# Optimization experiments

Hardware: AMD Instinct MI355X
Metric: run time of the kernel (lower is better)

The kernel has to match this reference:

```python
import math
import jax, jax.numpy as jnp
import numpy as np

B, S, D = 2, 2048, 4096
H, KVH = 32, 8
HD = D // H            # 128
REP = H // KVH         # 4


def setup_inputs() -> dict:
    key = jax.random.key(0)
    ks = jax.random.split(key, 7)
    scale = 1.0 / math.sqrt(D)
    return {
        "x": jax.random.normal(ks[0], (B, S, D), dtype=jnp.float32),
        "freqs_cos": jax.random.uniform(ks[1], (S, HD // 2), dtype=jnp.float32),
        "freqs_sin": jax.random.uniform(ks[2], (S, HD // 2), dtype=jnp.float32),
        "Wq": jax.random.normal(ks[3], (D, H * HD), dtype=jnp.float32) * scale,
        "Wk": jax.random.normal(ks[4], (D, KVH * HD), dtype=jnp.float32) * scale,
        "Wv": jax.random.normal(ks[5], (D, KVH * HD), dtype=jnp.float32) * scale,
        "Wo": jax.random.normal(ks[6], (H * HD, D), dtype=jnp.float32) * scale,
    }


def _rope(t, cos, sin):
    # t: [B,S,h,HD]; pairs are interleaved (reshape to (HD//2, 2) in original)
    tr = t[..., 0::2]
    ti = t[..., 1::2]
    cos = cos[None, :, None, :]  # [1,S,1,HD//2]
    sin = sin[None, :, None, :]
    out_r = tr * cos - ti * sin
    out_i = tr * sin + ti * cos
    return jnp.stack([out_r, out_i], axis=-1).reshape(t.shape)


def reference(x, freqs_cos, freqs_sin, Wq, Wk, Wv, Wo):
    b, s, _ = x.shape
    xq = (x @ Wq).reshape(b, s, H, HD)
    xk = (x @ Wk).reshape(b, s, KVH, HD)
    xv = (x @ Wv).reshape(b, s, KVH, HD)

    xq = _rope(xq, freqs_cos, freqs_sin)
    xk = _rope(xk, freqs_cos, freqs_sin)

    # GQA: repeat each kv head REP times -> [b,s,H,HD]
    xk = jnp.repeat(xk, REP, axis=2)
    xv = jnp.repeat(xv, REP, axis=2)

    q = xq.transpose(0, 2, 1, 3)  # [b,H,s,HD]
    k = xk.transpose(0, 2, 1, 3)
    v = xv.transpose(0, 2, 1, 3)

    scores = jnp.einsum('bhqd,bhkd->bhqk', q, k) / math.sqrt(HD)
    causal = jnp.tril(jnp.ones((s, s), dtype=bool))
    scores = jnp.where(causal[None, None], scores, jnp.float32(-jnp.inf))
    probs = jax.nn.softmax(scores.astype(jnp.float32), axis=-1).astype(x.dtype)

    out = jnp.einsum('bhqk,bhkd->bhqd', probs, v)
    out = out.transpose(0, 2, 1, 3).reshape(b, s, H * HD)
    return out @ Wo
```

## Files before the change

kernel.cpp:

```cpp
#include <hip/hip_runtime.h>

typedef unsigned short u16;
typedef unsigned int u32;
typedef __attribute__((ext_vector_type(8))) short bf16x8;
typedef __attribute__((ext_vector_type(8))) unsigned short u16x8;
typedef __attribute__((ext_vector_type(4))) unsigned short u16x4;
typedef __attribute__((ext_vector_type(4))) float f32x4;
typedef __attribute__((ext_vector_type(4))) unsigned int u32x4;

#define S_LEN 2048
#define NB 2
#define NH 32
#define NKVH 8
#define HD 128
#define DMODEL 4096
#define NEG_BIG (-1.0e30f)

__device__ __forceinline__ float bf2f(u16 x) {
  union { u32 u; float f; } v; v.u = ((u32)x) << 16; return v.f;
}
__device__ __forceinline__ u16 f2bf(float f) {
  union { float f; u32 u; } v; v.f = f;
  u32 r = v.u + 0x7FFFu + ((v.u >> 16) & 1u);
  return (u16)(r >> 16);
}

__device__ __forceinline__ void gload16(const void* g, void* l) {
  __builtin_amdgcn_global_load_lds(
      (const __attribute__((address_space(1))) void*)g,
      (__attribute__((address_space(3))) void*)l, 16, 0, 0);
}

__global__ __launch_bounds__(256) void convert_x(const float* __restrict__ x,
                                                 u16* __restrict__ xb)
{
  int i = blockIdx.x * 256 + threadIdx.x;
  f32x4 a = *(const f32x4*)&x[(size_t)i * 8];
  f32x4 b = *(const f32x4*)&x[(size_t)i * 8 + 4];
  u16x8 h = { f2bf(a[0]), f2bf(a[1]), f2bf(a[2]), f2bf(a[3]),
              f2bf(b[0]), f2bf(b[1]), f2bf(b[2]), f2bf(b[3]) };
  *(u16x8*)&xb[(size_t)i * 8] = h;
}

__global__ __launch_bounds__(256) void transpose_w(const float* __restrict__ W,
                                                   u16* __restrict__ out,
                                                   int N)
{
  __shared__ u16 Ls[64 * 68];
  const int t  = threadIdx.x;
  const int k0 = blockIdx.x * 64;
  const int n0 = blockIdx.y * 64;
#pragma unroll
  for (int i = 0; i < 4; ++i) {
    int kr = (t >> 4) + i * 16;
    int nc = (t & 15) * 4;
    f32x4 v = *(const f32x4*)&W[(size_t)(k0 + kr) * N + n0 + nc];
    u16x4 h = { f2bf(v[0]), f2bf(v[1]), f2bf(v[2]), f2bf(v[3]) };
    *(u16x4*)&Ls[kr * 68 + nc] = h;
  }
  __syncthreads();
#pragma unroll
  for (int i = 0; i < 2; ++i) {
    int nr = (t >> 3) + i * 32;
    int kc = (t & 7) * 8;
    u16x8 h;
#pragma unroll
    for (int j = 0; j < 8; ++j) h[j] = Ls[(kc + j) * 68 + nr];
    *(u16x8*)&out[(size_t)(n0 + nr) * 4096 + k0 + kc] = h;
  }
}

__global__ __launch_bounds__(256) void transpose_v(const u16* __restrict__ Yv,
                                                   u16* __restrict__ Vt)
{
  __shared__ u16 Ls[64 * 68];
  const int t  = threadIdx.x;
  const int s0 = blockIdx.x * 64;
  const int d0 = blockIdx.y * 64;
  const int z  = blockIdx.z;
#pragma unroll
  for (int i = 0; i < 2; ++i) {
    int sr = (t >> 3) + i * 32;
    int dc = (t & 7) * 8;
    u16x8 v = *(const u16x8*)&Yv[((size_t)(z >> 3) * S_LEN + s0 + sr) * 1024 +
                                 (z & 7) * 128 + d0 + dc];
    u16x4 lo = { v[0], v[1], v[2], v[3] };
    u16x4 hi = { v[4], v[5], v[6], v[7] };
    *(u16x4*)&Ls[sr * 68 + dc]     = lo;
    *(u16x4*)&Ls[sr * 68 + dc + 4] = hi;
  }
  __syncthreads();
#pragma unroll
  for (int i = 0; i < 2; ++i) {
    int dr = (t >> 3) + i * 32;
    int sc = (t & 7) * 8;
    u16x8 h;
#pragma unroll
    for (int j = 0; j < 8; ++j) h[j] = Ls[(sc + j) * 68 + dr];
    *(u16x8*)&Vt[((size_t)z * 128 + d0 + dr) * S_LEN + s0 + sc] = h;
  }
}

__global__ __launch_bounds__(256) void gemm_qkv(const u16* __restrict__ A,
                                                const u16* __restrict__ Bt,
                                                u16* __restrict__ Yq,
                                                u16* __restrict__ Yk,
                                                u16* __restrict__ Yv)
{
  __shared__ u16 As[128 * 64];
  __shared__ u16 Bs[128 * 64];
  const int tid  = threadIdx.x;
  const int wave = tid >> 6;
  const int lane = tid & 63;
  const int lr   = lane & 15;
  const int quad = lane >> 4;
  const int wm   = (wave >> 1) * 64;
  const int wn   = (wave & 1) * 64;
  const int bm   = blockIdx.y * 128;
  const int bn   = blockIdx.x * 128;

  const int col = (((lane & 7) ^ (lane >> 3)) * 8);
  const int r0  = wave * 32 + (lane >> 3);

  const f32x4 zero = {0.f, 0.f, 0.f, 0.f};
  f32x4 acc[4][4];
#pragma unroll
  for (int i = 0; i < 4; ++i)
#pragma unroll
    for (int j = 0; j < 4; ++j) acc[i][j] = zero;

  for (int kt = 0; kt < 4096; kt += 64) {
    __syncthreads();
#pragma unroll
    for (int c = 0; c < 4; ++c) {
      gload16(&A [(size_t)(bm + r0 + c * 8) * 4096 + kt + col],
              &As[wave * 2048 + c * 512]);
      gload16(&Bt[(size_t)(bn + r0 + c * 8) * 4096 + kt + col],
              &Bs[wave * 2048 + c * 512]);
    }
    __syncthreads();

#pragma unroll
    for (int kk = 0; kk < 2; ++kk) {
      bf16x8 af[4], bfr[4];
#pragma unroll
      for (int mt = 0; mt < 4; ++mt)
        af[mt] = *(const bf16x8*)&As[(wm + mt * 16 + lr) * 64 +
                                     (((kk * 4 + quad) ^ (lr & 7)) * 8)];
#pragma unroll
      for (int nt = 0; nt < 4; ++nt)
        bfr[nt] = *(const bf16x8*)&Bs[(wn + nt * 16 + lr) * 64 +
                                      (((kk * 4 + quad) ^ (lr & 7)) * 8)];
#pragma unroll
      for (int mt = 0; mt < 4; ++mt)
#pragma unroll
        for (int nt = 0; nt < 4; ++nt)
          acc[mt][nt] = __builtin_amdgcn_mfma_f32_16x16x32_bf16(af[mt], bfr[nt], acc[mt][nt], 0, 0, 0);
    }
  }

  u16* dst; size_t ldc; int nbase;
  if (bn < 4096)      { dst = Yq; ldc = 4096; nbase = bn; }
  else if (bn < 5120) { dst = Yk; ldc = 1024; nbase = bn - 4096; }
  else                { dst = Yv; ldc = 1024; nbase = bn - 5120; }
#pragma unroll
  for (int mt = 0; mt < 4; ++mt)
#pragma unroll
    for (int nt = 0; nt < 4; ++nt)
#pragma unroll
      for (int r = 0; r < 4; ++r) {
        size_t m = (size_t)(bm + wm + mt * 16 + quad * 4 + r);
        size_t n = (size_t)(nbase + wn + nt * 16 + lr);
        dst[m * ldc + n] = f2bf(acc[mt][nt][r]);
      }
}

__global__ __launch_bounds__(256) void gemm_o(const u16* __restrict__ A,
                                              const u16* __restrict__ Bt,
                                              float* __restrict__ C)
{
  __shared__ u16 As[128 * 64];
  __shared__ u16 Bs[128 * 64];
  const int tid  = threadIdx.x;
  const int wave = tid >> 6;
  const int lane = tid & 63;
  const int lr   = lane & 15;
  const int quad = lane >> 4;
  const int wm   = (wave >> 1) * 64;
  const int wn   = (wave & 1) * 64;
  const int bm   = blockIdx.y * 128;
  const int bn   = blockIdx.x * 128;

  const int col = (((lane & 7) ^ (lane >> 3)) * 8);
  const int r0  = wave * 32 + (lane >> 3);

  const f32x4 zero = {0.f, 0.f, 0.f, 0.f};
  f32x4 acc[4][4];
#pragma unroll
  for (int i = 0; i < 4; ++i)
#pragma unroll
    for (int j = 0; j < 4; ++j) acc[i][j] = zero;

  for (int kt = 0; kt < 4096; kt += 64) {
    __syncthreads();
#pragma unroll
    for (int c = 0; c < 4; ++c) {
      gload16(&A [(size_t)(bm + r0 + c * 8) * 4096 + kt + col],
              &As[wave * 2048 + c * 512]);
      gload16(&Bt[(size_t)(bn + r0 + c * 8) * 4096 + kt + col],
              &Bs[wave * 2048 + c * 512]);
    }
    __syncthreads();

#pragma unroll
    for (int kk = 0; kk < 2; ++kk) {
      bf16x8 af[4], bfr[4];
#pragma unroll
      for (int mt = 0; mt < 4; ++mt)
        af[mt] = *(const bf16x8*)&As[(wm + mt * 16 + lr) * 64 +
                                     (((kk * 4 + quad) ^ (lr & 7)) * 8)];
#pragma unroll
      for (int nt = 0; nt < 4; ++nt)
        bfr[nt] = *(const bf16x8*)&Bs[(wn + nt * 16 + lr) * 64 +
                                      (((kk * 4 + quad) ^ (lr & 7)) * 8)];
#pragma unroll
      for (int mt = 0; mt < 4; ++mt)
#pragma unroll
        for (int nt = 0; nt < 4; ++nt)
          acc[mt][nt] = __builtin_amdgcn_mfma_f32_16x16x32_bf16(af[mt], bfr[nt], acc[mt][nt], 0, 0, 0);
    }
  }

#pragma unroll
  for (int mt = 0; mt < 4; ++mt)
#pragma unroll
    for (int nt = 0; nt < 4; ++nt)
#pragma unroll
      for (int r = 0; r < 4; ++r) {
        size_t m = (size_t)(bm + wm + mt * 16 + quad * 4 + r);
        size_t n = (size_t)(bn + wn + nt * 16 + lr);
        C[m * 4096 + n] = acc[mt][nt][r];
      }
}

__global__ __launch_bounds__(256) void rope_v(u16* __restrict__ Y,
                                              const float* __restrict__ cp,
                                              const float* __restrict__ sp,
                                              int log2nh, int total)
{
  int g = blockIdx.x * 256 + threadIdx.x;
  if (g >= total) return;
  int j = (g & 15) * 4;
  int s = (g >> (4 + log2nh)) & (S_LEN - 1);
  u16x8 t = *(const u16x8*)&Y[(size_t)g * 8];
  f32x4 c  = *(const f32x4*)&cp[s * 64 + j];
  f32x4 sn = *(const f32x4*)&sp[s * 64 + j];
  u16x8 o;
#pragma unroll
  for (int p = 0; p < 4; ++p) {
    float tr = bf2f(t[2 * p]);
    float ti = bf2f(t[2 * p + 1]);
    o[2 * p]     = f2bf(tr * c[p] - ti * sn[p]);
    o[2 * p + 1] = f2bf(tr * sn[p] + ti * c[p]);
  }
  *(u16x8*)&Y[(size_t)g * 8] = o;
}

__global__ __launch_bounds__(512) void attn_kernel(const u16* Q,
                                                   const u16* __restrict__ K,
                                                   const u16* __restrict__ V,
                                                   u16* O)
{
  __shared__ u16 Ks[64 * 136];
  __shared__ u16 Vs[144 * 72];
  __shared__ u16 Ps[8 * 16 * 72];

  const int tid  = threadIdx.x;
  const int wave = tid >> 6;
  const int lane = tid & 63;
  const int lr   = lane & 15;
  const int quad = lane >> 4;

  const int b   = blockIdx.z;
  const int h   = blockIdx.y;
  const int q0  = ((int)gridDim.x - 1 - (int)blockIdx.x) * 128;
  const int kvh = h >> 2;

  for (int i = tid; i < 16 * 72; i += 512) {
    int dd = i / 72;
    Vs[(size_t)(128 + dd) * 72 + (i % 72)] = (dd == 0) ? (u16)0x3F80 : (u16)0;
  }

  const int wbase = q0 + wave * 16;
  const u16* qptr = Q + ((size_t)((b * S_LEN + wbase + lr) * NH + h)) * HD;
  bf16x8 aq[4];
#pragma unroll
  for (int c = 0; c < 4; ++c) aq[c] = *(const bf16x8*)(qptr + c * 32 + quad * 8);

  const f32x4 zero = {0.f, 0.f, 0.f, 0.f};
  f32x4 accO[9];
#pragma unroll
  for (int nt = 0; nt < 9; ++nt) accO[nt] = zero;
  float m_run[4];
#pragma unroll
  for (int r = 0; r < 4; ++r) m_run[r] = NEG_BIG;

  const float scale = 0.08838834764831845f;
  const int myq = wbase + quad * 4;

  int krow_[2], d0_[2], vd_[2], vk8_[2];
  size_t kbase[2], vbase[2];
#pragma unroll
  for (int i = 0; i < 2; ++i) {
    int e = (tid + i * 512) * 8;
    krow_[i] = e >> 7;
    d0_[i]   = e & 127;
    int cch = tid + i * 512;
    vd_[i]  = cch >> 3;
    vk8_[i] = cch & 7;
    kbase[i] = ((size_t)((b * S_LEN + krow_[i]) * NKVH + kvh)) * HD + d0_[i];
    vbase[i] = ((size_t)((b * NKVH + kvh) * HD + vd_[i])) * S_LEN + vk8_[i] * 8;
  }

  u32x4 kreg[2], vreg[2];
#pragma unroll
  for (int i = 0; i < 2; ++i) {
    kreg[i] = *(const u32x4*)&K[kbase[i]];
    vreg[i] = *(const u32x4*)&V[vbase[i]];
  }

  const int kv_end = q0 + 64;
  for (int kv0 = 0; kv0 <= kv_end; kv0 += 64) {
    const bool dg = (kv0 + 63 > wbase);
    __syncthreads();
#pragma unroll
    for (int i = 0; i < 2; ++i) {
      *(u32x4*)&Ks[krow_[i] * 136 + d0_[i]] = kreg[i];
      *(u32x4*)&Vs[vd_[i] * 72 + ((vk8_[i] * 8) ^ (((vd_[i] >> 3) & 7) << 3))] = vreg[i];
    }
    __syncthreads();

    if (kv0 + 64 <= kv_end) {
#pragma unroll
      for (int i = 0; i < 2; ++i) {
        kreg[i] = *(const u32x4*)&K[kbase[i] + (size_t)(kv0 + 64) * (NKVH * HD)];
        vreg[i] = *(const u32x4*)&V[vbase[i] + kv0 + 64];
      }
    }

    f32x4 sa[4];
    __builtin_amdgcn_s_setprio(1);
#pragma unroll
    for (int t = 0; t < 4; ++t) {
      f32x4 a = zero;
#pragma unroll
      for (int c = 0; c < 4; ++c) {
        bf16x8 bk = *(const bf16x8*)&Ks[(t * 16 + lr) * 136 + c * 32 + quad * 8];
        a = __builtin_amdgcn_mfma_f32_16x16x32_bf16(aq[c], bk, a, 0, 0, 0);
      }
      sa[t] = a;
    }
    __builtin_amdgcn_s_setprio(0);

    float alpha[4];
#pragma unroll
    for (int r = 0; r < 4; ++r) {
      const int row = myq + r;
      float s[4];
#pragma unroll
      for (int t = 0; t < 4; ++t) {
        float v = sa[t][r] * scale;
        if (dg) v = (kv0 + t * 16 + lr <= row) ? v : NEG_BIG;
        s[t] = v;
      }
      float mx = fmaxf(fmaxf(s[0], s[1]), fmaxf(s[2], s[3]));
#pragma unroll
      for (int off = 8; off >= 1; off >>= 1) mx = fmaxf(mx, __shfl_xor(mx, off));
      float mn = fmaxf(m_run[r], mx);
      alpha[r] = __expf(m_run[r] - mn);
      m_run[r] = mn;
      const int q  = quad * 4 + r;
      const int sw = (q & 7) << 3;
      const int base = wave * 1152 + q * 72;
#pragma unroll
      for (int t = 0; t < 4; ++t)
        Ps[base + ((t * 16 + lr) ^ sw)] = f2bf(__expf(s[t] - mn));
    }
#pragma unroll
    for (int nt = 0; nt < 9; ++nt)
#pragma unroll
      for (int r = 0; r < 4; ++r) accO[nt][r] *= alpha[r];

    __builtin_amdgcn_s_setprio(1);
#pragma unroll
    for (int kt2 = 0; kt2 < 2; ++kt2) {
      bf16x8 pf = *(const bf16x8*)&Ps[wave * 1152 + lr * 72 +
                                      ((kt2 * 32 + quad * 8) ^ ((lr & 7) << 3))];
#pragma unroll
      for (int nt = 0; nt < 9; ++nt) {
        const int d = nt * 16 + lr;
        bf16x8 vf = *(const bf16x8*)&Vs[d * 72 +
                                        ((kt2 * 32 + quad * 8) ^ (((d >> 3) & 7) << 3))];
        accO[nt] = __builtin_amdgcn_mfma_f32_16x16x32_bf16(pf, vf, accO[nt], 0, 0, 0);
      }
    }
    __builtin_amdgcn_s_setprio(0);
  }

  float rl[4];
#pragma unroll
  for (int r = 0; r < 4; ++r) {
    float l = __shfl(accO[8][r], lane & 48);
    rl[r] = 1.0f / l;
  }
#pragma unroll
  for (int nt = 0; nt < 8; ++nt)
#pragma unroll
    for (int r = 0; r < 4; ++r) {
      size_t q = (size_t)(wbase + quad * 4 + r);
      O[((size_t)b * S_LEN + q) * DMODEL + (size_t)h * HD + nt * 16 + lr] =
          f2bf(accO[nt][r] * rl[r]);
    }
}

extern "C" void kernel_launch(void* const* d_in, const int* in_sizes, int n_in,
                              void* d_out, int out_size, void* d_ws, size_t ws_size,
                              hipStream_t stream)
{
  const float* x  = (const float*)d_in[0];
  const float* cp = (const float*)d_in[1];
  const float* sp = (const float*)d_in[2];
  const float* Wq = (const float*)d_in[3];
  const float* Wk = (const float*)d_in[4];
  const float* Wv = (const float*)d_in[5];
  const float* Wo = (const float*)d_in[6];

  u16* Wt  = (u16*)d_ws;
  u16* Yq  = Wt + (size_t)25165824;
  u16* Yk  = Yq + (size_t)16777216;
  u16* Yv  = Yk + (size_t)4194304;
  u16* att = Yq;
  u16* WoT = Wt;
  u16* Vt  = Wt;
  u16* xb  = (u16*)d_out;

  transpose_w<<<dim3(64, 64), 256, 0, stream>>>(Wq, Wt,                    4096);
  transpose_w<<<dim3(64, 16), 256, 0, stream>>>(Wk, Wt + (size_t)4096*4096, 1024);
  transpose_w<<<dim3(64, 16), 256, 0, stream>>>(Wv, Wt + (size_t)5120*4096, 1024);
  convert_x<<<8192, 256, 0, stream>>>(x, xb);
  gemm_qkv<<<dim3(48, 32), 256, 0, stream>>>(xb, Wt, Yq, Yk, Yv);
  rope_v<<<8192, 256, 0, stream>>>(Yq, cp, sp, 5, 2097152);
  rope_v<<<2048, 256, 0, stream>>>(Yk, cp, sp, 3, 524288);
  transpose_v<<<dim3(32, 2, 16), 256, 0, stream>>>(Yv, Vt);
  attn_kernel<<<dim3(16, 32, 2), 512, 0, stream>>>(Yq, Yk, Vt, att);
  transpose_w<<<dim3(64, 64), 256, 0, stream>>>(Wo, WoT, 4096);
  gemm_o<<<dim3(32, 32), 256, 0, stream>>>(att, WoT, (float*)d_out);
}
```

Measured before the change: 933.1 us.

## Rewrite projection GEMMs with 256x128 tiles and triple-buffered LDS pipeline

Both projection GEMMs (QKV and output) are rebuilt on a shared body. Each block now uses 512 threads and a 256x128 output tile. The loop uses a three-stage LDS ring with direct global-to-LDS loads and a single barrier per K-step, gated by vmcnt waits, so loads overlap MFMA work. A flat grid is remapped with an XCD-aware block swizzle, and MFMA sections are wrapped in s_setprio. This aims to hide global-load latency and improve L2 reuse, at the cost of about 147KB of LDS per block, which limits occupancy to one block per CU.

```diff
diff --git a/kernel.cpp b/kernel.cpp
--- a/kernel.cpp
+++ b/kernel.cpp
@@ -101,68 +101,117 @@
   }
 }
 
-__global__ __launch_bounds__(256) void gemm_qkv(const u16* __restrict__ A,
+__device__ __forceinline__ void stage256(const u16* __restrict__ Ag,
+                                         const u16* __restrict__ Bg,
+                                         u16* as, u16* bs,
+                                         int bm, int bn, int kt, int tid)
+{
+  const int wave = tid >> 6;
+  const int rsub = tid >> 3;
+  const int col  = kt + (((tid & 7) ^ (rsub & 7)) * 8);
+#pragma unroll
+  for (int c = 0; c < 4; ++c)
+    gload16(&Ag[(size_t)(bm + c * 64 + rsub) * 4096 + col],
+            &as[c * 4096 + wave * 512]);
+#pragma unroll
+  for (int c = 0; c < 2; ++c)
+    gload16(&Bg[(size_t)(bn + c * 64 + rsub) * 4096 + col],
+            &bs[c * 4096 + wave * 512]);
+}
+
+#define GEMM256_BODY(Ag, Bg)                                                   \
+  __shared__ u16 As[3][16384];                                                 \
+  __shared__ u16 Bs[3][8192];                                                  \
+  const int tid  = threadIdx.x;                                                \
+  const int lane = tid & 63;                                                   \
+  const int lr   = lane & 15;                                                  \
+  const int quad = lane >> 4;                                                  \
+  const int wave = tid >> 6;                                                   \
+  const int wm   = (wave >> 1) * 64;                                           \
+  const int wn   = (wave & 1) * 64;                                            \
+  const int nwg  = (int)gridDim.x;                                             \
+  const int id   = (int)blockIdx.x;                                            \
+  const int swz  = (id & 7) * (nwg >> 3) + (id >> 3);                          \
+  const int by   = swz / NBX;                                                  \
+  const int bx   = swz - by * NBX;                                             \
+  const int bm   = by * 256;                                                   \
+  const int bn0  = bx * 128;                                                   \
+  const f32x4 zero = {0.f, 0.f, 0.f, 0.f};                                     \
+  f32x4 acc[4][4];                                                             \
+  _Pragma("unroll")                                                            \
+  for (int i = 0; i < 4; ++i)                                                  \
+    _Pragma("unroll")                                                          \
+    for (int j = 0; j < 4; ++j) acc[i][j] = zero;                              \
+  stage256(Ag, Bg, As[0], Bs[0], bm, bn0, 0,  tid);                            \
+  stage256(Ag, Bg, As[1], Bs[1], bm, bn0, 64, tid);                            \
+  for (int t = 0; t < 63; ++t) {                                               \
+    asm volatile("s_waitcnt vmcnt(6)" ::: "memory");                           \
+    __builtin_amdgcn_s_barrier();                                              \
+    if (t + 2 < 64)                                                            \
+      stage256(Ag, Bg, As[(t + 2) % 3], Bs[(t + 2) % 3], bm, bn0,              \
+               (t + 2) * 64, tid);                                             \
+    const u16* as = As[t % 3];                                                 \
+    const u16* bs = Bs[t % 3];                                                 \
+    _Pragma("unroll")                                                          \
+    for (int kk = 0; kk < 2; ++kk) {                                           \
+      bf16x8 af[4], bfr[4];                                                    \
+      _Pragma("unroll")                                                        \
+      for (int mt = 0; mt < 4; ++mt)                                           \
+        af[mt] = *(const bf16x8*)&as[(wm + mt * 16 + lr) * 64 +                \
+                                     (((kk * 4 + quad) ^ (lr & 7)) * 8)];      \
+      _Pragma("unroll")                                                        \
+      for (int nt = 0; nt < 4; ++nt)                                           \
+        bfr[nt] = *(const bf16x8*)&bs[(wn + nt * 16 + lr) * 64 +               \
+                                      (((kk * 4 + quad) ^ (lr & 7)) * 8)];     \
+      __builtin_amdgcn_s_setprio(1);                                           \
+      _Pragma("unroll")                                                        \
+      for (int mt = 0; mt < 4; ++mt)                                           \
+        _Pragma("unroll")                                                      \
+        for (int nt = 0; nt < 4; ++nt)                                         \
+          acc[mt][nt] = __builtin_amdgcn_mfma_f32_16x16x32_bf16(               \
+              af[mt], bfr[nt], acc[mt][nt], 0, 0, 0);                          \
+      __builtin_amdgcn_s_setprio(0);                                           \
+    }                                                                          \
+  }                                                                            \
+  asm volatile("s_waitcnt vmcnt(0)" ::: "memory");                             \
+  __builtin_amdgcn_s_barrier();                                                \
+  {                                                                            \
+    const u16* as = As[0];                                    \
+    const u16* bs = Bs[0];                                                     \
+    _Pragma("unroll")                                                          \
+    for (int kk = 0; kk < 2; ++kk) {                                           \
+      bf16x8 af[4], bfr[4];                                                    \
+      _Pragma("unroll")                                                        \
+      for (int mt = 0; mt < 4; ++mt)                                           \
+        af[mt] = *(const bf16x8*)&as[(wm + mt * 16 + lr) * 64 +                \
+                                     (((kk * 4 + quad) ^ (lr & 7)) * 8)];      \
+      _Pragma("unroll")                                                        \
+      for (int nt = 0; nt < 4; ++nt)                                           \
+        bfr[nt] = *(const bf16x8*)&bs[(wn + nt * 16 + lr) * 64 +               \
+                                      (((kk * 4 + quad) ^ (lr & 7)) * 8)];     \
+      __builtin_amdgcn_s_setprio(1);                                           \
+      _Pragma("unroll")                                                        \
+      for (int mt = 0; mt < 4; ++mt)                                           \
+        _Pragma("unroll")                                                      \
+        for (int nt = 0; nt < 4; ++nt)                                         \
+          acc[mt][nt] = __builtin_amdgcn_mfma_f32_16x16x32_bf16(               \
+              af[mt], bfr[nt], acc[mt][nt], 0, 0, 0);                          \
+      __builtin_amdgcn_s_setprio(0);                                           \
+    }                                                                          \
+  }
+
+__global__ __launch_bounds__(512) void gemm_qkv(const u16* __restrict__ A,
                                                 const u16* __restrict__ Bt,
                                                 u16* __restrict__ Yq,
                                                 u16* __restrict__ Yk,
                                                 u16* __restrict__ Yv)
 {
-  __shared__ u16 As[128 * 64];
-  __shared__ u16 Bs[128 * 64];
-  const int tid  = threadIdx.x;
-  const int wave = tid >> 6;
-  const int lane = tid & 63;
-  const int lr   = lane & 15;
-  const int quad = lane >> 4;
-  const int wm   = (wave >> 1) * 64;
-  const int wn   = (wave & 1) * 64;
-  const int bm   = blockIdx.y * 128;
-  const int bn   = blockIdx.x * 128;
-
-  const int col = (((lane & 7) ^ (lane >> 3)) * 8);
-  const int r0  = wave * 32 + (lane >> 3);
-
-  const f32x4 zero = {0.f, 0.f, 0.f, 0.f};
-  f32x4 acc[4][4];
-#pragma unroll
-  for (int i = 0; i < 4; ++i)
-#pragma unroll
-    for (int j = 0; j < 4; ++j) acc[i][j] = zero;
-
-  for (int kt = 0; kt < 4096; kt += 64) {
-    __syncthreads();
-#pragma unroll
-    for (int c = 0; c < 4; ++c) {
-      gload16(&A [(size_t)(bm + r0 + c * 8) * 4096 + kt + col],
-              &As[wave * 2048 + c * 512]);
-      gload16(&Bt[(size_t)(bn + r0 + c * 8) * 4096 + kt + col],
-              &Bs[wave * 2048 + c * 512]);
-    }
-    __syncthreads();
-
-#pragma unroll
-    for (int kk = 0; kk < 2; ++kk) {
-      bf16x8 af[4], bfr[4];
-#pragma unroll
-      for (int mt = 0; mt < 4; ++mt)
-        af[mt] = *(const bf16x8*)&As[(wm + mt * 16 + lr) * 64 +
-                                     (((kk * 4 + quad) ^ (lr & 7)) * 8)];
-#pragma unroll
-      for (int nt = 0; nt < 4; ++nt)
-        bfr[nt] = *(const bf16x8*)&Bs[(wn + nt * 16 + lr) * 64 +
-                                      (((kk * 4 + quad) ^ (lr & 7)) * 8)];
-#pragma unroll
-      for (int mt = 0; mt < 4; ++mt)
-#pragma unroll
-        for (int nt = 0; nt < 4; ++nt)
-          acc[mt][nt] = __builtin_amdgcn_mfma_f32_16x16x32_bf16(af[mt], bfr[nt], acc[mt][nt], 0, 0, 0);
-    }
-  }
-
+  const int NBX = 48;
+  GEMM256_BODY(A, Bt)
   u16* dst; size_t ldc; int nbase;
-  if (bn < 4096)      { dst = Yq; ldc = 4096; nbase = bn; }
-  else if (bn < 5120) { dst = Yk; ldc = 1024; nbase = bn - 4096; }
-  else                { dst = Yv; ldc = 1024; nbase = bn - 5120; }
+  if (bn0 < 4096)      { dst = Yq; ldc = 4096; nbase = bn0; }
+  else if (bn0 < 5120) { dst = Yk; ldc = 1024; nbase = bn0 - 4096; }
+  else                 { dst = Yv; ldc = 1024; nbase = bn0 - 5120; }
 #pragma unroll
   for (int mt = 0; mt < 4; ++mt)
 #pragma unroll
@@ -175,62 +224,12 @@
       }
 }
 
-__global__ __launch_bounds__(256) void gemm_o(const u16* __restrict__ A,
+__global__ __launch_bounds__(512) void gemm_o(const u16* __restrict__ A,
                                               const u16* __restrict__ Bt,
                                               float* __restrict__ C)
 {
-  __shared__ u16 As[128 * 64];
-  __shared__ u16 Bs[128 * 64];
-  const int tid  = threadIdx.x;
-  const int wave = tid >> 6;
-  const int lane = tid & 63;
-  const int lr   = lane & 15;
-  const int quad = lane >> 4;
-  const int wm   = (wave >> 1) * 64;
-  const int wn   = (wave & 1) * 64;
-  const int bm   = blockIdx.y * 128;
-  const int bn   = blockIdx.x * 128;
-
-  const int col = (((lane & 7) ^ (lane >> 3)) * 8);
-  const int r0  = wave * 32 + (lane >> 3);
-
-  const f32x4 zero = {0.f, 0.f, 0.f, 0.f};
-  f32x4 acc[4][4];
-#pragma unroll
-  for (int i = 0; i < 4; ++i)
-#pragma unroll
-    for (int j = 0; j < 4; ++j) acc[i][j] = zero;
-
-  for (int kt = 0; kt < 4096; kt += 64) {
-    __syncthreads();
-#pragma unroll
-    for (int c = 0; c < 4; ++c) {
-      gload16(&A [(size_t)(bm + r0 + c * 8) * 4096 + kt + col],
-              &As[wave * 2048 + c * 512]);
-      gload16(&Bt[(size_t)(bn + r0 + c * 8) * 4096 + kt + col],
-              &Bs[wave * 2048 + c * 512]);
-    }
-    __syncthreads();
-
-#pragma unroll
-    for (int kk = 0; kk < 2; ++kk) {
-      bf16x8 af[4], bfr[4];
-#pragma unroll
-      for (int mt = 0; mt < 4; ++mt)
-        af[mt] = *(const bf16x8*)&As[(wm + mt * 16 + lr) * 64 +
-                                     (((kk * 4 + quad) ^ (lr & 7)) * 8)];
-#pragma unroll
-      for (int nt = 0; nt < 4; ++nt)
-        bfr[nt] = *(const bf16x8*)&Bs[(wn + nt * 16 + lr) * 64 +
-                                      (((kk * 4 + quad) ^ (lr & 7)) * 8)];
-#pragma unroll
-      for (int mt = 0; mt < 4; ++mt)
-#pragma unroll
-        for (int nt = 0; nt < 4; ++nt)
-          acc[mt][nt] = __builtin_amdgcn_mfma_f32_16x16x32_bf16(af[mt], bfr[nt], acc[mt][nt], 0, 0, 0);
-    }
-  }
-
+  const int NBX = 32;
+  GEMM256_BODY(A, Bt)
 #pragma unroll
   for (int mt = 0; mt < 4; ++mt)
 #pragma unroll
@@ -238,7 +237,7 @@
 #pragma unroll
       for (int r = 0; r < 4; ++r) {
         size_t m = (size_t)(bm + wm + mt * 16 + quad * 4 + r);
-        size_t n = (size_t)(bn + wn + nt * 16 + lr);
+        size_t n = (size_t)(bn0 + wn + nt * 16 + lr);
         C[m * 4096 + n] = acc[mt][nt][r];
       }
 }
@@ -448,11 +447,11 @@
   transpose_w<<<dim3(64, 16), 256, 0, stream>>>(Wk, Wt + (size_t)4096*4096, 1024);
   transpose_w<<<dim3(64, 16), 256, 0, stream>>>(Wv, Wt + (size_t)5120*4096, 1024);
   convert_x<<<8192, 256, 0, stream>>>(x, xb);
-  gemm_qkv<<<dim3(48, 32), 256, 0, stream>>>(xb, Wt, Yq, Yk, Yv);
+  gemm_qkv<<<768, 512, 0, stream>>>(xb, Wt, Yq, Yk, Yv);
   rope_v<<<8192, 256, 0, stream>>>(Yq, cp, sp, 5, 2097152);
   rope_v<<<2048, 256, 0, stream>>>(Yk, cp, sp, 3, 524288);
   transpose_v<<<dim3(32, 2, 16), 256, 0, stream>>>(Yv, Vt);
   attn_kernel<<<dim3(16, 32, 2), 512, 0, stream>>>(Yq, Yk, Vt, att);
   transpose_w<<<dim3(64, 64), 256, 0, stream>>>(Wo, WoT, 4096);
-  gemm_o<<<dim3(32, 32), 256, 0, stream>>>(att, WoT, (float*)d_out);
-}
+  gemm_o<<<512, 512, 0, stream>>>(att, WoT, (float*)d_out);
+}
```

After: 987.8 us. 1.06x slower.
